# Kernel optimization log

Hardware: AMD Instinct MI355X
Metric: run time of the kernel (lower is better)

## Reference

```python
import jax, jax.numpy as jnp
import numpy as np

N = 100000      # nodes
E = 1600000     # edges
F_IN = 27       # node features
EMB = 64        # embedding size
H = 128         # hidden/out channels
L = 4           # GNN layers
G = 512         # num_graphs


def setup_inputs() -> dict:
    key = jax.random.key(0)
    ks = jax.random.split(key, 13)
    s = 0.05
    return {
        "x": jax.random.normal(ks[0], (N, F_IN), jnp.float32),
        "edge_index": jax.random.randint(ks[1], (2, E), 0, N),
        "batch": jnp.sort(jax.random.randint(ks[2], (N,), 0, G)),
        "lin0_w": jax.random.normal(ks[3], (F_IN, EMB), jnp.float32) * s,
        "ggc_weight": jax.random.normal(ks[4], (L, H, H), jnp.float32) * s,
        "gru_w_ih": jax.random.normal(ks[5], (3 * H, H), jnp.float32) * s,
        "gru_w_hh": jax.random.normal(ks[6], (3 * H, H), jnp.float32) * s,
        "gru_b_ih": jax.random.normal(ks[7], (3 * H,), jnp.float32) * s,
        "gru_b_hh": jax.random.normal(ks[8], (3 * H,), jnp.float32) * s,
        "lin1_w": jax.random.normal(ks[9], (H, 1), jnp.float32) * s,
        "lin1_b": jax.random.normal(ks[10], (1,), jnp.float32) * s,
        "lin2_w": jax.random.normal(ks[11], (H, 1), jnp.float32) * s,
        "lin2_b": jax.random.normal(ks[12], (1,), jnp.float32) * s,
    }


def _gru_cell(m, h, w_ih, w_hh, b_ih, b_hh):
    # torch.nn.GRUCell math
    gi = m @ w_ih.T + b_ih          # [N, 3H]
    gh = h @ w_hh.T + b_hh          # [N, 3H]
    i_r, i_z, i_n = jnp.split(gi, 3, axis=1)
    h_r, h_z, h_n = jnp.split(gh, 3, axis=1)
    r = jax.nn.sigmoid(i_r + h_r)
    z = jax.nn.sigmoid(i_z + h_z)
    n = jnp.tanh(i_n + r * h_n)
    return (1.0 - z) * n + z * h


def reference(x, edge_index, batch, lin0_w, ggc_weight,
              gru_w_ih, gru_w_hh, gru_b_ih, gru_b_hh,
              lin1_w, lin1_b, lin2_w, lin2_b):
    x1 = jax.nn.sigmoid(x @ lin0_w)                       # [N, EMB]
    h = jnp.pad(x1, ((0, 0), (0, H - EMB)))               # pad to out_channels
    src, dst = edge_index[0], edge_index[1]
    for i in range(L):
        m = h @ ggc_weight[i]                             # [N, H]
        m = jax.ops.segment_sum(m[src], dst, num_segments=N)  # add-aggregate at target
        h = _gru_cell(m, h, gru_w_ih, gru_w_hh, gru_b_ih, gru_b_hh)
    xr = jax.nn.relu(h)
    mu = xr @ lin1_w + lin1_b                             # [N, 1]
    sigma = jax.nn.softplus(xr @ lin2_w + lin2_b)         # [N, 1]
    uncorrected_mu = mu
    mu_all = jax.ops.segment_sum(mu, batch, num_segments=G)        # [G, 1]
    sigma_all = jax.ops.segment_sum(sigma, batch, num_segments=G)  # [G, 1]
    # vectorized per-graph correction (original loops over graphs)
    mu_c = mu - mu_all[batch] * (sigma / sigma_all[batch])
    return (mu_c.squeeze(1), x1, sigma.squeeze(1), uncorrected_mu.squeeze(1))
```

## Files before the change

kernel.cpp:

```cpp
#include <hip/hip_runtime.h>
#include <math.h>

#define NN 100000
#define FIN 27
#define EMB 64
#define HH 128
#define LAYERS 4
#define GG 512
#define SCAN_CHUNK 2048
#define SPAN 512
#define SPANSHIFT 9
#define MAXNB 256
#define ECAP 16384
#define LPAD_US 136

typedef __attribute__((ext_vector_type(8))) short short8;
typedef __attribute__((ext_vector_type(4))) float floatx4;

__device__ __forceinline__ float sigmf(float x) { return 1.0f / (1.0f + __expf(-x)); }
__device__ __forceinline__ float tanhfast(float x) { return 1.0f - 2.0f / (__expf(2.0f * x) + 1.0f); }

__device__ __forceinline__ unsigned short f2bf(float f) {
    unsigned int u = __float_as_uint(f);
    u += 0x7FFFu + ((u >> 16) & 1u);
    return (unsigned short)(u >> 16);
}

__device__ __forceinline__ float bflo(unsigned int v) { return __uint_as_float(v << 16); }
__device__ __forceinline__ float bfhi(unsigned int v) { return __uint_as_float(v & 0xFFFF0000u); }
__device__ __forceinline__ float bfs(unsigned short v) { return __uint_as_float(((unsigned)v) << 16); }

__global__ __launch_bounds__(256)
void lin0_kernel(const float* __restrict__ x, const float* __restrict__ w,
                 float* __restrict__ x1_out, unsigned short* __restrict__ hbf, int n) {
    int gwave = (int)((blockIdx.x * blockDim.x + threadIdx.x) >> 6);
    int lane = threadIdx.x & 63;
    int nwaves = (int)((gridDim.x * blockDim.x) >> 6);
    float wreg[FIN];
#pragma unroll
    for (int k = 0; k < FIN; ++k) wreg[k] = w[k * EMB + lane];
    for (int i = gwave; i < n; i += nwaves) {
        float xv = (lane < FIN) ? x[(size_t)i * FIN + lane] : 0.0f;
        float acc = 0.0f;
#pragma unroll
        for (int k = 0; k < FIN; ++k) acc += __shfl(xv, k, 64) * wreg[k];
        float v = 1.0f / (1.0f + expf(-acc));
        x1_out[(size_t)i * EMB + lane] = v;
        hbf[(size_t)i * HH + lane] = f2bf(v);
    }
}

__global__ void bucket_scatter_direct(const int* __restrict__ src, const int* __restrict__ dst,
                                      int* __restrict__ bucket_cnt, unsigned* __restrict__ ebuf,
                                      int e) {
    __shared__ int lh[MAXNB];
    __shared__ int gb[MAXNB];
    int t = threadIdx.x;
    for (int i = t; i < MAXNB; i += 1024) lh[i] = 0;
    __syncthreads();
    int base = blockIdx.x * 8192;
    int lidx[8], sv[8], dv[8];
#pragma unroll
    for (int i = 0; i < 8; ++i) {
        int eid = base + i * 1024 + t;
        if (eid < e) {
            sv[i] = src[eid];
            dv[i] = dst[eid];
            lidx[i] = atomicAdd(&lh[dv[i] >> SPANSHIFT], 1);
        } else lidx[i] = -1;
    }
    __syncthreads();
    for (int i = t; i < MAXNB; i += 1024) {
        int c = lh[i];
        gb[i] = c ? atomicAdd(&bucket_cnt[i], c) : 0;
    }
    __syncthreads();
#pragma unroll
    for (int i = 0; i < 8; ++i) {
        if (lidx[i] >= 0) {
            int b = dv[i] >> SPANSHIFT;
            int pos = gb[b] + lidx[i];
            if (pos < ECAP) {
                unsigned dl = (unsigned)(dv[i] - (b << SPANSHIFT));
                ebuf[(size_t)b * ECAP + pos] = (dl << 17) | (unsigned)sv[i];
            }
        }
    }
}

__global__ void deg_from_buckets(const unsigned* __restrict__ ebuf, const int* __restrict__ bucket_cnt,
                                 int* __restrict__ deg, int n) {
    __shared__ int ld[SPAN];
    int b = blockIdx.x, t = threadIdx.x;
    ld[t] = 0; ld[t + 256] = 0;
    __syncthreads();
    int cnt = bucket_cnt[b];
    if (cnt > ECAP) cnt = ECAP;
    size_t base = (size_t)b * ECAP;
    int nodebase = b << SPANSHIFT;
    for (int j = t; j < cnt; j += 256)
        atomicAdd(&ld[ebuf[base + j] >> 17], 1);
    __syncthreads();
    int i0 = nodebase + t, i1 = nodebase + 256 + t;
    if (i0 < n) deg[i0] = ld[t];
    if (i1 < n) deg[i1] = ld[t + 256];
}

__global__ void scan_partial(const int* __restrict__ deg, int* __restrict__ blocksum, int n) {
    int b = blockIdx.x, t = threadIdx.x;
    int base = b * SCAN_CHUNK + t * 8;
    int s = 0;
#pragma unroll
    for (int i = 0; i < 8; ++i) {
        int idx = base + i;
        if (idx < n) s += deg[idx];
    }
#pragma unroll
    for (int off = 32; off > 0; off >>= 1) s += __shfl_down(s, off, 64);
    __shared__ int ws[4];
    if ((t & 63) == 0) ws[t >> 6] = s;
    __syncthreads();
    if (t == 0) blocksum[b] = ws[0] + ws[1] + ws[2] + ws[3];
}

__global__ void scan_blocksums(const int* __restrict__ blocksum, int* __restrict__ blockoff, int nb) {
    int t = threadIdx.x;
    int own = (t < nb) ? blocksum[t] : 0;
    int v = own;
    for (int off = 1; off < 64; off <<= 1) {
        int u = __shfl_up(v, off, 64);
        if (t >= off) v += u;
    }
    if (t < nb) blockoff[t] = v - own;
}

__global__ void scan_final(const int* __restrict__ deg, const int* __restrict__ blockoff,
                           int* __restrict__ rowptr, int n) {
    int b = blockIdx.x, t = threadIdx.x;
    int base = b * SCAN_CHUNK + t * 8;
    int v[8];
    int s = 0;
#pragma unroll
    for (int i = 0; i < 8; ++i) {
        int idx = base + i;
        v[i] = (idx < n) ? deg[idx] : 0;
        s += v[i];
    }
    __shared__ int ts[256];
    ts[t] = s;
    __syncthreads();
    for (int off = 1; off < 256; off <<= 1) {
        int u = (t >= off) ? ts[t - off] : 0;
        __syncthreads();
        ts[t] += u;
        __syncthreads();
    }
    int run = blockoff[b] + ((t == 0) ? 0 : ts[t - 1]);
#pragma unroll
    for (int i = 0; i < 8; ++i) {
        int idx = base + i;
        if (idx < n) {
            rowptr[idx] = run;
            run += v[i];
        } else if (idx == n) {
            rowptr[n] = run;
        }
    }
}

__global__ void place_kernel(const unsigned* __restrict__ ebuf, const int* __restrict__ bucket_cnt,
                             const int* __restrict__ rowptr, int* __restrict__ col, int n) {
    __shared__ int cur[SPAN];
    int b = blockIdx.x, t = threadIdx.x;
    int nodebase = b << SPANSHIFT;
    int i0 = nodebase + t, i1 = nodebase + 256 + t;
    cur[t] = (i0 < n) ? rowptr[i0] : 0;
    cur[t + 256] = (i1 < n) ? rowptr[i1] : 0;
    __syncthreads();
    int cnt = bucket_cnt[b];
    if (cnt > ECAP) cnt = ECAP;
    size_t base = (size_t)b * ECAP;
    for (int j = t; j < cnt; j += 256) {
        unsigned ed = ebuf[base + j];
        int pos = atomicAdd(&cur[ed >> 17], 1);
        col[pos] = (int)(ed & 0x1FFFFu);
    }
}

__global__ void pack_whh(const float* __restrict__ w_hh, unsigned short* __restrict__ whhp) {
    int id = blockIdx.x * blockDim.x + threadIdx.x;
    if (id >= 4 * 24 * 64 * 8) return;
    int j = id & 7;
    int lane = (id >> 3) & 63;
    int ctkt = id >> 9;
    int ct = ctkt % 24;
    int kt = ctkt / 24;
    int k = kt * 32 + (lane >> 4) * 8 + j;
    int col = ct * 16 + (lane & 15);
    whhp[id] = f2bf(w_hh[col * HH + k]);
}

__global__ void pack_wf(const float* __restrict__ ggc, const float* __restrict__ w_ih,
                        unsigned short* __restrict__ Wfp) {
    int id = blockIdx.x * blockDim.x + threadIdx.x;
    if (id >= LAYERS * 4 * 24 * 64 * 8) return;
    int l = id / 49152;
    int rem = id % 49152;
    int j = rem & 7;
    int lane = (rem >> 3) & 63;
    int ctkt = rem >> 9;
    int ct = ctkt % 24;
    int kt = ctkt / 24;
    int k = kt * 32 + (lane >> 4) * 8 + j;
    int col = ct * 16 + (lane & 15);
    const float4* gr = (const float4*)(ggc + ((size_t)l * HH + k) * HH);
    const float4* wr = (const float4*)(w_ih + (size_t)col * HH);
    float acc = 0.0f;
#pragma unroll 4
    for (int q = 0; q < HH / 4; ++q) {
        float4 g = gr[q], w = wr[q];
        acc += g.x * w.x + g.y * w.y + g.z * w.z + g.w * w.w;
    }
    Wfp[id] = f2bf(acc);
}

template <int HALF>
__global__ __launch_bounds__(512)
void layer_kernel(const unsigned short* __restrict__ hin,
                  unsigned short* __restrict__ hout,
                  const int* __restrict__ rowptr, const int* __restrict__ col,
                  const unsigned short* __restrict__ Wfp,
                  const unsigned short* __restrict__ whhp,
                  const float* __restrict__ b_ih, const float* __restrict__ b_hh,
                  int n) {
    __shared__ unsigned short aggL[16 * LPAD_US];
    __shared__ unsigned short hL[16 * LPAD_US];
    int wave = threadIdx.x >> 6;
    int lane = threadIdx.x & 63;
    int quad = lane >> 4;
    int l15 = lane & 15;
    int lg = quad, l16 = l15;
    int M0 = blockIdx.x * 16;
    if (M0 >= n) return;
    const uint4* hin4 = (const uint4*)hin;
    const uint2* hin2 = (const uint2*)hin;

    if (threadIdx.x < 256) {
        int row = threadIdx.x >> 4;
        int q = threadIdx.x & 15;
        if (M0 + row < n) {
            uint4 v;
            if (HALF && q >= 8) v = make_uint4(0, 0, 0, 0);
            else v = hin4[(size_t)(M0 + row) * 16 + q];
            *(uint4*)(&hL[row * LPAD_US + q * 8]) = v;
            if (HALF && q >= 8) *(uint4*)(&aggL[row * LPAD_US + q * 8]) = make_uint4(0, 0, 0, 0);
        }
    }

    int nb2 = M0 + wave * 2;
    int rp;
    {
        int idx = nb2 + lane;
        if (lane > 2 || idx > n) idx = n;
        rp = rowptr[idx];
    }

    for (int i = 0; i < 2; ++i) {
        int node = nb2 + i;
        int r0 = __shfl(rp, i, 64);
        int r1 = __shfl(rp, i + 1, 64);
        if (node >= n) r1 = r0;
        if (HALF) {
            float a[4], b[4];
#pragma unroll
            for (int k = 0; k < 4; ++k) { a[k] = 0.0f; b[k] = 0.0f; }
            int j = r0 + lg;
            for (; j + 4 < r1; j += 8) {
                int s0 = col[j], s1 = col[j + 4];
                uint2 v0 = hin2[(size_t)s0 * 32 + l16];
                uint2 v1 = hin2[(size_t)s1 * 32 + l16];
                a[0] += bflo(v0.x); a[1] += bfhi(v0.x);
                a[2] += bflo(v0.y); a[3] += bfhi(v0.y);
                b[0] += bflo(v1.x); b[1] += bfhi(v1.x);
                b[2] += bflo(v1.y); b[3] += bfhi(v1.y);
            }
            for (; j < r1; j += 4) {
                int s = col[j];
                uint2 v = hin2[(size_t)s * 32 + l16];
                a[0] += bflo(v.x); a[1] += bfhi(v.x);
                a[2] += bflo(v.y); a[3] += bfhi(v.y);
            }
#pragma unroll
            for (int k = 0; k < 4; ++k) {
                a[k] += b[k];
                a[k] += __shfl_xor(a[k], 32, 64);
                a[k] += __shfl_xor(a[k], 16, 64);
            }
            if (lg == 0 && node < n) {
                uint2 o;
                o.x = (unsigned)f2bf(a[0]) | ((unsigned)f2bf(a[1]) << 16);
                o.y = (unsigned)f2bf(a[2]) | ((unsigned)f2bf(a[3]) << 16);
                *(uint2*)(&aggL[(wave * 2 + i) * LPAD_US + l16 * 4]) = o;
            }
        } else {
            float a[8], b[8];
#pragma unroll
            for (int k = 0; k < 8; ++k) { a[k] = 0.0f; b[k] = 0.0f; }
            int j = r0 + lg;
            for (; j + 12 < r1; j += 16) {
                int s0 = col[j], s1 = col[j + 4], s2 = col[j + 8], s3 = col[j + 12];
                uint4 v0 = hin4[(size_t)s0 * 16 + l16];
                uint4 v1 = hin4[(size_t)s1 * 16 + l16];
                uint4 v2 = hin4[(size_t)s2 * 16 + l16];
                uint4 v3 = hin4[(size_t)s3 * 16 + l16];
                a[0] += bflo(v0.x); a[1] += bfhi(v0.x);
                a[2] += bflo(v0.y); a[3] += bfhi(v0.y);
                a[4] += bflo(v0.z); a[5] += bfhi(v0.z);
                a[6] += bflo(v0.w); a[7] += bfhi(v0.w);
                b[0] += bflo(v1.x); b[1] += bfhi(v1.x);
                b[2] += bflo(v1.y); b[3] += bfhi(v1.y);
                b[4] += bflo(v1.z); b[5] += bfhi(v1.z);
                b[6] += bflo(v1.w); b[7] += bfhi(v1.w);
                a[0] += bflo(v2.x); a[1] += bfhi(v2.x);
                a[2] += bflo(v2.y); a[3] += bfhi(v2.y);
                a[4] += bflo(v2.z); a[5] += bfhi(v2.z);
                a[6] += bflo(v2.w); a[7] += bfhi(v2.w);
                b[0] += bflo(v3.x); b[1] += bfhi(v3.x);
                b[2] += bflo(v3.y); b[3] += bfhi(v3.y);
                b[4] += bflo(v3.z); b[5] += bfhi(v3.z);
                b[6] += bflo(v3.w); b[7] += bfhi(v3.w);
            }
            for (; j + 4 < r1; j += 8) {
                int s0 = col[j], s1 = col[j + 4];
                uint4 v0 = hin4[(size_t)s0 * 16 + l16];
                uint4 v1 = hin4[(size_t)s1 * 16 + l16];
                a[0] += bflo(v0.x); a[1] += bfhi(v0.x);
                a[2] += bflo(v0.y); a[3] += bfhi(v0.y);
                a[4] += bflo(v0.z); a[5] += bfhi(v0.z);
                a[6] += bflo(v0.w); a[7] += bfhi(v0.w);
                b[0] += bflo(v1.x); b[1] += bfhi(v1.x);
                b[2] += bflo(v1.y); b[3] += bfhi(v1.y);
                b[4] += bflo(v1.z); b[5] += bfhi(v1.z);
                b[6] += bflo(v1.w); b[7] += bfhi(v1.w);
            }
            for (; j < r1; j += 4) {
                int s = col[j];
                uint4 v = hin4[(size_t)s * 16 + l16];
                a[0] += bflo(v.x); a[1] += bfhi(v.x);
                a[2] += bflo(v.y); a[3] += bfhi(v.y);
                a[4] += bflo(v.z); a[5] += bfhi(v.z);
                a[6] += bflo(v.w); a[7] += bfhi(v.w);
            }
#pragma unroll
            for (int k = 0; k < 8; ++k) {
                a[k] += b[k];
                a[k] += __shfl_xor(a[k], 32, 64);
                a[k] += __shfl_xor(a[k], 16, 64);
            }
            if (lg == 0 && node < n) {
                uint4 o;
                o.x = (unsigned)f2bf(a[0]) | ((unsigned)f2bf(a[1]) << 16);
                o.y = (unsigned)f2bf(a[2]) | ((unsigned)f2bf(a[3]) << 16);
                o.z = (unsigned)f2bf(a[4]) | ((unsigned)f2bf(a[5]) << 16);
                o.w = (unsigned)f2bf(a[6]) | ((unsigned)f2bf(a[7]) << 16);
                *(uint4*)(&aggL[(wave * 2 + i) * LPAD_US + l16 * 8]) = o;
            }
        }
    }

    __syncthreads();

    floatx4 acc_gi[3];
    floatx4 acc_gh[3];
#pragma unroll
    for (int g = 0; g < 3; ++g) {
        acc_gi[g] = (floatx4)0.0f;
        acc_gh[g] = (floatx4)0.0f;
    }

    const int KTMAX = HALF ? 2 : 4;
#pragma unroll
    for (int kt = 0; kt < KTMAX; ++kt) {
        int kbase = kt * 32 + quad * 8;
        int lrow = l15 * LPAD_US + kbase;
        short8 a_a = *(const short8*)(&aggL[lrow]);
        short8 a_h = *(const short8*)(&hL[lrow]);
#pragma unroll
        for (int g = 0; g < 3; ++g) {
            int ct = g * 8 + wave;
            size_t boff = ((size_t)(kt * 24 + ct) * 64 + lane) * 8;
            short8 bi = *(const short8*)(Wfp + boff);
            short8 bh = *(const short8*)(whhp + boff);
            acc_gi[g] = __builtin_amdgcn_mfma_f32_16x16x32_bf16(a_a, bi, acc_gi[g], 0, 0, 0);
            acc_gh[g] = __builtin_amdgcn_mfma_f32_16x16x32_bf16(a_h, bh, acc_gh[g], 0, 0, 0);
        }
    }

    __syncthreads();

    {
        int c = wave * 16 + l15;
        float bir = b_ih[c], biz = b_ih[128 + c], bin_ = b_ih[256 + c];
        float bhr = b_hh[c], bhz = b_hh[128 + c], bhn = b_hh[256 + c];
#pragma unroll
        for (int j = 0; j < 4; ++j) {
            int nl = quad * 4 + j;
            int lidx = nl * LPAD_US + c;
            float gir = acc_gi[0][j] + bir;
            float ghr = acc_gh[0][j] + bhr;
            float giz = acc_gi[1][j] + biz;
            float ghz = acc_gh[1][j] + bhz;
            float gin = acc_gi[2][j] + bin_;
            float ghn = acc_gh[2][j] + bhn;
            float rr = sigmf(gir + ghr);
            float zz = sigmf(giz + ghz);
            float nn = tanhfast(gin + rr * ghn);
            float hp = bfs(hL[lidx]);
            aggL[lidx] = f2bf((1.0f - zz) * nn + zz * hp);
        }
    }

    __syncthreads();

    if (threadIdx.x < 256) {
        int row = threadIdx.x >> 4;
        int q = threadIdx.x & 15;
        if (M0 + row < n) {
            uint4 v = *(const uint4*)(&aggL[row * LPAD_US + q * 8]);
            *(uint4*)(hout + (size_t)(M0 + row) * HH + q * 8) = v;
        }
    }
}

__global__ void readout_kernel(const unsigned int* __restrict__ h2, const float* __restrict__ w1,
                               const float* __restrict__ b1, const float* __restrict__ w2,
                               const float* __restrict__ b2,
                               float* __restrict__ out_mu, float* __restrict__ out_sg, int n) {
    int wave = (int)((blockIdx.x * blockDim.x + threadIdx.x) >> 6);
    int lane = threadIdx.x & 63;
    if (wave >= n) return;
    unsigned int u = h2[(size_t)wave * 64 + lane];
    float x0 = fmaxf(bflo(u), 0.0f);
    float x1 = fmaxf(bfhi(u), 0.0f);
    float2 wv1 = ((const float2*)w1)[lane];
    float2 wv2 = ((const float2*)w2)[lane];
    float a1 = x0 * wv1.x + x1 * wv1.y;
    float a2 = x0 * wv2.x + x1 * wv2.y;
#pragma unroll
    for (int off = 32; off > 0; off >>= 1) {
        a1 += __shfl_down(a1, off, 64);
        a2 += __shfl_down(a2, off, 64);
    }
    if (lane == 0) {
        float mu = a1 + b1[0];
        float x2 = a2 + b2[0];
        float sg = (x2 > 20.0f) ? x2 : __logf(1.0f + __expf(x2));
        out_mu[wave] = mu;
        out_sg[wave] = sg;
    }
}

__device__ __forceinline__ int lbound(const int* __restrict__ a, int n, int v) {
    int lo = 0, hi = n;
    while (lo < hi) {
        int m = (lo + hi) >> 1;
        if (a[m] < v) lo = m + 1; else hi = m;
    }
    return lo;
}

__global__ void seg_correct_kernel(const float* __restrict__ out_mu, const float* __restrict__ out_sg,
                                   const int* __restrict__ batch, float* __restrict__ out_muc, int n) {
    int g = blockIdx.x;
    int lo = lbound(batch, n, g);
    int hi = lbound(batch, n, g + 1);
    float smu = 0.0f, ssg = 0.0f;
    for (int i = lo + threadIdx.x; i < hi; i += blockDim.x) {
        smu += out_mu[i];
        ssg += out_sg[i];
    }
#pragma unroll
    for (int off = 32; off > 0; off >>= 1) {
        smu += __shfl_down(smu, off, 64);
        ssg += __shfl_down(ssg, off, 64);
    }
    __shared__ float pm[4], ps[4];
    int wave = threadIdx.x >> 6;
    int lane = threadIdx.x & 63;
    if (lane == 0) { pm[wave] = smu; ps[wave] = ssg; }
    __syncthreads();
    float tot_mu = pm[0] + pm[1] + pm[2] + pm[3];
    float tot_sg = ps[0] + ps[1] + ps[2] + ps[3];
    for (int i = lo + threadIdx.x; i < hi; i += blockDim.x) {
        out_muc[i] = out_mu[i] - tot_mu * (out_sg[i] / tot_sg);
    }
}

extern "C" void kernel_launch(void* const* d_in, const int* in_sizes, int n_in,
                              void* d_out, int out_size, void* d_ws, size_t ws_size,
                              hipStream_t stream) {
    const float* x      = (const float*)d_in[0];
    const int*   ei     = (const int*)d_in[1];
    const int*   batch  = (const int*)d_in[2];
    const float* lin0_w = (const float*)d_in[3];
    const float* ggc    = (const float*)d_in[4];
    const float* w_ih   = (const float*)d_in[5];
    const float* w_hh   = (const float*)d_in[6];
    const float* b_ih   = (const float*)d_in[7];
    const float* b_hh   = (const float*)d_in[8];
    const float* l1w    = (const float*)d_in[9];
    const float* l1b    = (const float*)d_in[10];
    const float* l2w    = (const float*)d_in[11];
    const float* l2b    = (const float*)d_in[12];

    int n = in_sizes[0] / FIN;
    int e = in_sizes[1] / 2;
    const int* src = ei;
    const int* dstp = ei + e;

    float* out = (float*)d_out;
    float* out_muc = out;
    float* out_x1  = out + n;
    float* out_sg  = out + n + (size_t)n * EMB;
    float* out_mu  = out_sg + n;

    unsigned short* hbf0 = (unsigned short*)d_ws;
    unsigned short* hbf1 = hbf0 + (size_t)n * HH;
    unsigned short* Wfp  = hbf1 + (size_t)n * HH;
    unsigned short* whhp = Wfp + (size_t)LAYERS * 49152;
    int*            deg      = (int*)(whhp + 49152 + 8);
    int*            rowptr   = deg + n;
    int*            blocksum = rowptr + n + 1;
    int*            blockoff = blocksum + 64;
    int*            bucket_cnt = blockoff + 64;
    int*            col      = bucket_cnt + MAXNB;
    unsigned*       ebuf     = (unsigned*)hbf1;

    int nbuck = (n + SPAN - 1) >> SPANSHIFT;
    hipMemsetAsync(bucket_cnt, 0, MAXNB * sizeof(int), stream);

    lin0_kernel<<<2048, 256, 0, stream>>>(x, lin0_w, out_x1, hbf0, n);

    int eb = (e + 8191) / 8192;
    bucket_scatter_direct<<<eb, 1024, 0, stream>>>(src, dstp, bucket_cnt, ebuf, e);
    deg_from_buckets<<<nbuck, 256, 0, stream>>>(ebuf, bucket_cnt, deg, n);

    int nb = (n + SCAN_CHUNK) / SCAN_CHUNK;
    scan_partial<<<nb, 256, 0, stream>>>(deg, blocksum, n);
    scan_blocksums<<<1, 64, 0, stream>>>(blocksum, blockoff, nb);
    scan_final<<<nb, 256, 0, stream>>>(deg, blockoff, rowptr, n);

    place_kernel<<<nbuck, 256, 0, stream>>>(ebuf, bucket_cnt, rowptr, col, n);

    pack_whh<<<(49152 + 255) / 256, 256, 0, stream>>>(w_hh, whhp);
    pack_wf<<<(LAYERS * 49152 + 255) / 256, 256, 0, stream>>>(ggc, w_ih, Wfp);

    int gru_blocks = (n + 15) / 16;
    unsigned short* hin = hbf0;
    unsigned short* hout = hbf1;
    for (int l = 0; l < LAYERS; ++l) {
        if (l == 0) {
            layer_kernel<1><<<gru_blocks, 512, 0, stream>>>(hin, hout, rowptr, col,
                                                            Wfp, whhp, b_ih, b_hh, n);
        } else {
            layer_kernel<0><<<gru_blocks, 512, 0, stream>>>(hin, hout, rowptr, col,
                                                            Wfp + (size_t)l * 49152, whhp,
                                                            b_ih, b_hh, n);
        }
        unsigned short* t = hin; hin = hout; hout = t;
    }

    int wave_blocks = (n * 64 + 255) / 256;
    readout_kernel<<<wave_blocks, 256, 0, stream>>>((const unsigned int*)hin, l1w, l1b, l2w, l2b,
                                                    out_mu, out_sg, n);
    seg_correct_kernel<<<GG, 256, 0, stream>>>(out_mu, out_sg, batch, out_muc, n);
}
```

Baseline: 615.1 us.

## Process 32 nodes per layer block and store byte offsets in col

Each layer block now covers 32 rows instead of 16. Every wave aggregates 4 nodes and issues two MFMA row tiles per loaded weight fragment, so each Wfp/whhp load is reused twice and the block count halves. The place kernel now writes byte offsets (node<<8) into col, which removes the per-gather multiply and shift. The cost is more registers per wave and more LDS per block, which may lower occupancy. The 32-bit offset encoding is still safe because N*256 fits in an int.

```diff
diff --git a/kernel.cpp b/kernel.cpp
--- a/kernel.cpp
+++ b/kernel.cpp
@@ -13,6 +13,7 @@
 #define MAXNB 256
 #define ECAP 16384
 #define LPAD_US 136
+#define TMB 32
 
 typedef __attribute__((ext_vector_type(8))) short short8;
 typedef __attribute__((ext_vector_type(4))) float floatx4;
@@ -183,7 +184,7 @@
     for (int j = t; j < cnt; j += 256) {
         unsigned ed = ebuf[base + j];
         int pos = atomicAdd(&cur[ed >> 17], 1);
-        col[pos] = (int)(ed & 0x1FFFFu);
+        col[pos] = (int)((ed & 0x1FFFFu) << 8);
     }
 }
 
@@ -233,40 +234,39 @@
                   const unsigned short* __restrict__ whhp,
                   const float* __restrict__ b_ih, const float* __restrict__ b_hh,
                   int n) {
-    __shared__ unsigned short aggL[16 * LPAD_US];
-    __shared__ unsigned short hL[16 * LPAD_US];
+    __shared__ unsigned short aggL[TMB * LPAD_US];
+    __shared__ unsigned short hL[TMB * LPAD_US];
     int wave = threadIdx.x >> 6;
     int lane = threadIdx.x & 63;
     int quad = lane >> 4;
     int l15 = lane & 15;
     int lg = quad, l16 = l15;
-    int M0 = blockIdx.x * 16;
+    int M0 = blockIdx.x * TMB;
     if (M0 >= n) return;
-    const uint4* hin4 = (const uint4*)hin;
-    const uint2* hin2 = (const uint2*)hin;
-
-    if (threadIdx.x < 256) {
+    const char* hinb = (const char*)hin;
+
+    {
         int row = threadIdx.x >> 4;
         int q = threadIdx.x & 15;
         if (M0 + row < n) {
             uint4 v;
             if (HALF && q >= 8) v = make_uint4(0, 0, 0, 0);
-            else v = hin4[(size_t)(M0 + row) * 16 + q];
+            else v = ((const uint4*)hin)[(size_t)(M0 + row) * 16 + q];
             *(uint4*)(&hL[row * LPAD_US + q * 8]) = v;
             if (HALF && q >= 8) *(uint4*)(&aggL[row * LPAD_US + q * 8]) = make_uint4(0, 0, 0, 0);
         }
     }
 
-    int nb2 = M0 + wave * 2;
+    int nb4 = M0 + wave * 4;
     int rp;
     {
-        int idx = nb2 + lane;
-        if (lane > 2 || idx > n) idx = n;
+        int idx = nb4 + lane;
+        if (lane > 4 || idx > n) idx = n;
         rp = rowptr[idx];
     }
 
-    for (int i = 0; i < 2; ++i) {
-        int node = nb2 + i;
+    for (int i = 0; i < 4; ++i) {
+        int node = nb4 + i;
         int r0 = __shfl(rp, i, 64);
         int r1 = __shfl(rp, i + 1, 64);
         if (node >= n) r1 = r0;
@@ -276,17 +276,17 @@
             for (int k = 0; k < 4; ++k) { a[k] = 0.0f; b[k] = 0.0f; }
             int j = r0 + lg;
             for (; j + 4 < r1; j += 8) {
-                int s0 = col[j], s1 = col[j + 4];
-                uint2 v0 = hin2[(size_t)s0 * 32 + l16];
-                uint2 v1 = hin2[(size_t)s1 * 32 + l16];
+                int o0 = col[j], o1 = col[j + 4];
+                uint2 v0 = *(const uint2*)(hinb + o0 + l16 * 8);
+                uint2 v1 = *(const uint2*)(hinb + o1 + l16 * 8);
                 a[0] += bflo(v0.x); a[1] += bfhi(v0.x);
                 a[2] += bflo(v0.y); a[3] += bfhi(v0.y);
                 b[0] += bflo(v1.x); b[1] += bfhi(v1.x);
                 b[2] += bflo(v1.y); b[3] += bfhi(v1.y);
             }
             for (; j < r1; j += 4) {
-                int s = col[j];
-                uint2 v = hin2[(size_t)s * 32 + l16];
+                int o = col[j];
+                uint2 v = *(const uint2*)(hinb + o + l16 * 8);
                 a[0] += bflo(v.x); a[1] += bfhi(v.x);
                 a[2] += bflo(v.y); a[3] += bfhi(v.y);
             }
@@ -300,7 +300,7 @@
                 uint2 o;
                 o.x = (unsigned)f2bf(a[0]) | ((unsigned)f2bf(a[1]) << 16);
                 o.y = (unsigned)f2bf(a[2]) | ((unsigned)f2bf(a[3]) << 16);
-                *(uint2*)(&aggL[(wave * 2 + i) * LPAD_US + l16 * 4]) = o;
+                *(uint2*)(&aggL[(wave * 4 + i) * LPAD_US + l16 * 4]) = o;
             }
         } else {
             float a[8], b[8];
@@ -308,11 +308,11 @@
             for (int k = 0; k < 8; ++k) { a[k] = 0.0f; b[k] = 0.0f; }
             int j = r0 + lg;
             for (; j + 12 < r1; j += 16) {
-                int s0 = col[j], s1 = col[j + 4], s2 = col[j + 8], s3 = col[j + 12];
-                uint4 v0 = hin4[(size_t)s0 * 16 + l16];
-                uint4 v1 = hin4[(size_t)s1 * 16 + l16];
-                uint4 v2 = hin4[(size_t)s2 * 16 + l16];
-                uint4 v3 = hin4[(size_t)s3 * 16 + l16];
+                int o0 = col[j], o1 = col[j + 4], o2 = col[j + 8], o3 = col[j + 12];
+                uint4 v0 = *(const uint4*)(hinb + o0 + l16 * 16);
+                uint4 v1 = *(const uint4*)(hinb + o1 + l16 * 16);
+                uint4 v2 = *(const uint4*)(hinb + o2 + l16 * 16);
+                uint4 v3 = *(const uint4*)(hinb + o3 + l16 * 16);
                 a[0] += bflo(v0.x); a[1] += bfhi(v0.x);
                 a[2] += bflo(v0.y); a[3] += bfhi(v0.y);
                 a[4] += bflo(v0.z); a[5] += bfhi(v0.z);
@@ -331,9 +331,9 @@
                 b[6] += bflo(v3.w); b[7] += bfhi(v3.w);
             }
             for (; j + 4 < r1; j += 8) {
-                int s0 = col[j], s1 = col[j + 4];
-                uint4 v0 = hin4[(size_t)s0 * 16 + l16];
-                uint4 v1 = hin4[(size_t)s1 * 16 + l16];
+                int o0 = col[j], o1 = col[j + 4];
+                uint4 v0 = *(const uint4*)(hinb + o0 + l16 * 16);
+                uint4 v1 = *(const uint4*)(hinb + o1 + l16 * 16);
                 a[0] += bflo(v0.x); a[1] += bfhi(v0.x);
                 a[2] += bflo(v0.y); a[3] += bfhi(v0.y);
                 a[4] += bflo(v0.z); a[5] += bfhi(v0.z);
@@ -344,8 +344,8 @@
                 b[6] += bflo(v1.w); b[7] += bfhi(v1.w);
             }
             for (; j < r1; j += 4) {
-                int s = col[j];
-                uint4 v = hin4[(size_t)s * 16 + l16];
+                int o = col[j];
+                uint4 v = *(const uint4*)(hinb + o + l16 * 16);
                 a[0] += bflo(v.x); a[1] += bfhi(v.x);
                 a[2] += bflo(v.y); a[3] += bfhi(v.y);
                 a[4] += bflo(v.z); a[5] += bfhi(v.z);
@@ -363,36 +363,40 @@
                 o.y = (unsigned)f2bf(a[2]) | ((unsigned)f2bf(a[3]) << 16);
                 o.z = (unsigned)f2bf(a[4]) | ((unsigned)f2bf(a[5]) << 16);
                 o.w = (unsigned)f2bf(a[6]) | ((unsigned)f2bf(a[7]) << 16);
-                *(uint4*)(&aggL[(wave * 2 + i) * LPAD_US + l16 * 8]) = o;
-            }
-        }
-    }
-
-    __syncthreads();
-
-    floatx4 acc_gi[3];
-    floatx4 acc_gh[3];
-#pragma unroll
-    for (int g = 0; g < 3; ++g) {
-        acc_gi[g] = (floatx4)0.0f;
-        acc_gh[g] = (floatx4)0.0f;
-    }
+                *(uint4*)(&aggL[(wave * 4 + i) * LPAD_US + l16 * 8]) = o;
+            }
+        }
+    }
+
+    __syncthreads();
+
+    floatx4 gi[2][3], gh[2][3];
+#pragma unroll
+    for (int m = 0; m < 2; ++m)
+#pragma unroll
+        for (int g = 0; g < 3; ++g) {
+            gi[m][g] = (floatx4)0.0f;
+            gh[m][g] = (floatx4)0.0f;
+        }
 
     const int KTMAX = HALF ? 2 : 4;
 #pragma unroll
     for (int kt = 0; kt < KTMAX; ++kt) {
         int kbase = kt * 32 + quad * 8;
-        int lrow = l15 * LPAD_US + kbase;
-        short8 a_a = *(const short8*)(&aggL[lrow]);
-        short8 a_h = *(const short8*)(&hL[lrow]);
+        short8 aA0 = *(const short8*)(&aggL[l15 * LPAD_US + kbase]);
+        short8 aH0 = *(const short8*)(&hL[l15 * LPAD_US + kbase]);
+        short8 aA1 = *(const short8*)(&aggL[(16 + l15) * LPAD_US + kbase]);
+        short8 aH1 = *(const short8*)(&hL[(16 + l15) * LPAD_US + kbase]);
 #pragma unroll
         for (int g = 0; g < 3; ++g) {
             int ct = g * 8 + wave;
             size_t boff = ((size_t)(kt * 24 + ct) * 64 + lane) * 8;
             short8 bi = *(const short8*)(Wfp + boff);
             short8 bh = *(const short8*)(whhp + boff);
-            acc_gi[g] = __builtin_amdgcn_mfma_f32_16x16x32_bf16(a_a, bi, acc_gi[g], 0, 0, 0);
-            acc_gh[g] = __builtin_amdgcn_mfma_f32_16x16x32_bf16(a_h, bh, acc_gh[g], 0, 0, 0);
+            gi[0][g] = __builtin_amdgcn_mfma_f32_16x16x32_bf16(aA0, bi, gi[0][g], 0, 0, 0);
+            gi[1][g] = __builtin_amdgcn_mfma_f32_16x16x32_bf16(aA1, bi, gi[1][g], 0, 0, 0);
+            gh[0][g] = __builtin_amdgcn_mfma_f32_16x16x32_bf16(aH0, bh, gh[0][g], 0, 0, 0);
+            gh[1][g] = __builtin_amdgcn_mfma_f32_16x16x32_bf16(aH1, bh, gh[1][g], 0, 0, 0);
         }
     }
 
@@ -403,26 +407,29 @@
         float bir = b_ih[c], biz = b_ih[128 + c], bin_ = b_ih[256 + c];
         float bhr = b_hh[c], bhz = b_hh[128 + c], bhn = b_hh[256 + c];
 #pragma unroll
-        for (int j = 0; j < 4; ++j) {
-            int nl = quad * 4 + j;
-            int lidx = nl * LPAD_US + c;
-            float gir = acc_gi[0][j] + bir;
-            float ghr = acc_gh[0][j] + bhr;
-            float giz = acc_gi[1][j] + biz;
-            float ghz = acc_gh[1][j] + bhz;
-            float gin = acc_gi[2][j] + bin_;
-            float ghn = acc_gh[2][j] + bhn;
-            float rr = sigmf(gir + ghr);
-            float zz = sigmf(giz + ghz);
-            float nn = tanhfast(gin + rr * ghn);
-            float hp = bfs(hL[lidx]);
-            aggL[lidx] = f2bf((1.0f - zz) * nn + zz * hp);
-        }
-    }
-
-    __syncthreads();
-
-    if (threadIdx.x < 256) {
+        for (int m = 0; m < 2; ++m) {
+#pragma unroll
+            for (int j = 0; j < 4; ++j) {
+                int row = m * 16 + quad * 4 + j;
+                int lidx = row * LPAD_US + c;
+                float gir = gi[m][0][j] + bir;
+                float ghr = gh[m][0][j] + bhr;
+                float giz = gi[m][1][j] + biz;
+                float ghz = gh[m][1][j] + bhz;
+                float gin = gi[m][2][j] + bin_;
+                float ghn = gh[m][2][j] + bhn;
+                float rr = sigmf(gir + ghr);
+                float zz = sigmf(giz + ghz);
+                float nn = tanhfast(gin + rr * ghn);
+                float hp = bfs(hL[lidx]);
+                aggL[lidx] = f2bf((1.0f - zz) * nn + zz * hp);
+            }
+        }
+    }
+
+    __syncthreads();
+
+    {
         int row = threadIdx.x >> 4;
         int q = threadIdx.x & 15;
         if (M0 + row < n) {
@@ -555,17 +562,17 @@
     pack_whh<<<(49152 + 255) / 256, 256, 0, stream>>>(w_hh, whhp);
     pack_wf<<<(LAYERS * 49152 + 255) / 256, 256, 0, stream>>>(ggc, w_ih, Wfp);
 
-    int gru_blocks = (n + 15) / 16;
+    int layer_blocks = (n + TMB - 1) / TMB;
     unsigned short* hin = hbf0;
     unsigned short* hout = hbf1;
     for (int l = 0; l < LAYERS; ++l) {
         if (l == 0) {
-            layer_kernel<1><<<gru_blocks, 512, 0, stream>>>(hin, hout, rowptr, col,
-                                                            Wfp, whhp, b_ih, b_hh, n);
+            layer_kernel<1><<<layer_blocks, 512, 0, stream>>>(hin, hout, rowptr, col,
+                                                              Wfp, whhp, b_ih, b_hh, n);
         } else {
-            layer_kernel<0><<<gru_blocks, 512, 0, stream>>>(hin, hout, rowptr, col,
-                                                            Wfp + (size_t)l * 49152, whhp,
-                                                            b_ih, b_hh, n);
+            layer_kernel<0><<<layer_blocks, 512, 0, stream>>>(hin, hout, rowptr, col,
+                                                              Wfp + (size_t)l * 49152, whhp,
+                                                              b_ih, b_hh, n);
         }
         unsigned short* t = hin; hin = hout; hout = t;
     }
```

Result: slower. 663.9 us (+7.9%).
